# Kernel tuning notes

Measured on AMD Instinct MI355X. Metric: run time of the kernel, lower is better.

## Reference

```python
import jax, jax.numpy as jnp
import numpy as np

B, S, E, H = 4, 8192, 1024, 16
D = E // H  # head_dim = 64


def setup_inputs() -> dict:
    key = jax.random.key(0)
    ks = jax.random.split(key, 9)
    s = 0.02
    return {
        "x": jax.random.normal(ks[0], (B, S, E), dtype=jnp.float32),
        "Wq": jax.random.normal(ks[1], (D, E), dtype=jnp.float32) * s,
        "bq": jax.random.normal(ks[2], (D,), dtype=jnp.float32) * s,
        "Wk": jax.random.normal(ks[3], (D, E), dtype=jnp.float32) * s,
        "bk": jax.random.normal(ks[4], (D,), dtype=jnp.float32) * s,
        "Wv": jax.random.normal(ks[5], (D, E), dtype=jnp.float32) * s,
        "bv": jax.random.normal(ks[6], (D,), dtype=jnp.float32) * s,
        "Wo": jax.random.normal(ks[7], (E, E), dtype=jnp.float32) * s,
        "bo": jax.random.normal(ks[8], (E,), dtype=jnp.float32) * s,
    }


def reference(x, Wq, bq, Wk, bk, Wv, bv, Wo, bo):
    b, s, e = x.shape
    d = Wq.shape[0]          # head_dim (projections map embed_dim -> head_dim)
    h = e // d               # num_heads
    # torch Linear: y = x @ W.T + b ; projected shape [B, S, d]
    # view(B, -1, h, d) on [B, S, d] => effective seq S' = S // h (faithful to source)
    def split_heads(t):
        return t.reshape(b, -1, h, d).transpose(0, 2, 1, 3)  # [B, H, S', D]
    q = split_heads(x @ Wq.T + bq)
    k = split_heads(x @ Wk.T + bk)
    v = split_heads(x @ Wv.T + bv)
    scores = jnp.einsum('bhqd,bhkd->bhqk', q, k) / np.sqrt(d).astype(jnp.float32)
    attn = jax.nn.softmax(scores, axis=-1)  # dropout=0.0 => identity
    ctx = jnp.einsum('bhqk,bhkd->bhqd', attn, v)
    ctx = ctx.transpose(0, 2, 1, 3).reshape(b, -1, e)  # [B, S', E]
    return ctx @ Wo.T + bo
```

## Files before the change

kernel.cpp:

```cpp
#include <hip/hip_runtime.h>
#include <hip/hip_bf16.h>


typedef unsigned short u16;
typedef __attribute__((ext_vector_type(8))) short short8;
typedef __attribute__((ext_vector_type(4))) float f32x4;

#define VMWAIT(N) asm volatile("s_waitcnt vmcnt(" #N ")" ::: "memory")
#define MEMFENCE() asm volatile("" ::: "memory")
#define BAR() __builtin_amdgcn_s_barrier()

__device__ inline u16 f2bf(float f) {
    union { float f; unsigned u; } v; v.f = f;
    unsigned u = v.u;
    return (u16)((u + 0x7fffu + ((u >> 16) & 1u)) >> 16);
}
__device__ inline unsigned pack_bf2(float a, float b) {
    union { __hip_bfloat162 h; unsigned u; } v;
    v.h = __float22bfloat162_rn(float2{a, b});
    return v.u;
}
__device__ __forceinline__ void gld16(void* lds, const void* gptr) {
    __builtin_amdgcn_global_load_lds(
        (const __attribute__((address_space(1))) unsigned int*)gptr,
        (__attribute__((address_space(3))) unsigned int*)lds,
        16, 0, 0);
}

__global__ __launch_bounds__(256) void convw(
    const float* __restrict__ Wq, const float* __restrict__ bq,
    const float* __restrict__ Wk, const float* __restrict__ bk,
    const float* __restrict__ Wv, const float* __restrict__ bv,
    const float* __restrict__ Wo,
    u16* __restrict__ Wqkv, float* __restrict__ qkvb, u16* __restrict__ Wob)
{
    const int idx = blockIdx.x * 256 + threadIdx.x;
    Wob[idx] = f2bf(Wo[idx]);
    if (idx < 196608) {
        const int row = idx >> 10, k = idx & 1023;
        float v = (row < 64)  ? Wq[row * 1024 + k] * 0.125f
                : (row < 128) ? Wk[(row - 64) * 1024 + k]
                              : Wv[(row - 128) * 1024 + k];
        Wqkv[idx] = f2bf(v);
    }
    if (idx < 192) {
        qkvb[idx] = (idx < 64) ? bq[idx] * 0.125f
                  : (idx < 128) ? bk[idx - 64] : bv[idx - 128];
    }
}

__global__ __launch_bounds__(256) void qkv_gemm(
    const float* __restrict__ X, const u16* __restrict__ W,
    const float* __restrict__ bias, u16* __restrict__ Out)
{
    __shared__ short8 Bs[2][1536];

    const int tid = threadIdx.x;
    const int lane = tid & 63, wid = tid >> 6;
    const int q = lane >> 4, r = lane & 15;
    const long m0 = (long)blockIdx.x * 64;

    const u16* wp[6];
    #pragma unroll
    for (int i = 0; i < 6; ++i) {
        const int p = wid * 6 + i, kk2 = p / 12, nt = p % 12;
        wp[i] = W + (long)(nt * 16 + r) * 1024 + kk2 * 32 + q * 8;
    }

    const float* px = X + (m0 + wid * 16 + r) * 1024 + q * 8;

    f32x4 acc[12] = {};

    #pragma unroll
    for (int i = 0; i < 6; ++i)
        gld16(&Bs[0][(wid * 6 + i) * 64], wp[i]);
    float4 a[4];
    a[0] = *(const float4*)(px);
    a[1] = *(const float4*)(px + 4);
    a[2] = *(const float4*)(px + 32);
    a[3] = *(const float4*)(px + 36);

    for (int k0 = 0; k0 < 1024; k0 += 64) {
        const int buf = (k0 >> 6) & 1;
        float4 an[4] = {};
        if (k0 + 64 < 1024) {
            #pragma unroll
            for (int i = 0; i < 6; ++i)
                gld16(&Bs[buf ^ 1][(wid * 6 + i) * 64], wp[i] + k0 + 64);
            an[0] = *(const float4*)(px + k0 + 64);
            an[1] = *(const float4*)(px + k0 + 68);
            an[2] = *(const float4*)(px + k0 + 96);
            an[3] = *(const float4*)(px + k0 + 100);
            VMWAIT(10);
        } else {
            VMWAIT(0);
        }
        BAR();
        MEMFENCE();
        #pragma unroll
        for (int kk2 = 0; kk2 < 2; ++kk2) {
            union { short8 s; unsigned u[4]; } af;
            af.u[0] = pack_bf2(a[kk2 * 2].x, a[kk2 * 2].y);
            af.u[1] = pack_bf2(a[kk2 * 2].z, a[kk2 * 2].w);
            af.u[2] = pack_bf2(a[kk2 * 2 + 1].x, a[kk2 * 2 + 1].y);
            af.u[3] = pack_bf2(a[kk2 * 2 + 1].z, a[kk2 * 2 + 1].w);
            #pragma unroll
            for (int nt = 0; nt < 12; ++nt)
                acc[nt] = __builtin_amdgcn_mfma_f32_16x16x32_bf16(
                    af.s, Bs[buf][(kk2 * 12 + nt) * 64 + lane], acc[nt], 0, 0, 0);
        }
        MEMFENCE();
        BAR();
        #pragma unroll
        for (int i = 0; i < 4; ++i) a[i] = an[i];
    }

    u16* reg = (u16*)(&Bs[0][0]) + wid * 3072;
    #pragma unroll
    for (int nt = 0; nt < 12; ++nt) {
        const float badd = bias[nt * 16 + r];
        #pragma unroll
        for (int e = 0; e < 4; ++e)
            reg[(q * 4 + e) * 192 + nt * 16 + r] = f2bf(acc[nt][e] + badd);
    }
    asm volatile("s_waitcnt lgkmcnt(0)" ::: "memory");
    u16* ob = Out + (m0 + wid * 16) * 192;
    #pragma unroll
    for (int t = 0; t < 6; ++t) {
        short8 v = *(const short8*)(reg + t * 512 + lane * 8);
        *(short8*)(ob + t * 512 + lane * 8) = v;
    }
}

__global__ __launch_bounds__(256) void vtrans(
    const u16* __restrict__ qkv, u16* __restrict__ Vt)
{
    __shared__ u16 T[64][68];
    const int bh = blockIdx.x, b = bh >> 4, h = bh & 15;
    const int i0 = blockIdx.y * 64;
    const int tid = threadIdx.x;

    #pragma unroll
    for (int it = 0; it < 2; ++it) {
        const int c = tid + 256 * it;
        const int il = c >> 3, d8 = (c & 7) * 8;
        short8 v = *(const short8*)(qkv +
            ((long)b * 8192 + (long)(i0 + il) * 16 + h) * 192 + 128 + d8);
        #pragma unroll
        for (int j = 0; j < 8; ++j) T[d8 + j][il] = (u16)v[j];
    }
    __syncthreads();
    #pragma unroll
    for (int it = 0; it < 2; ++it) {
        const int c = tid + 256 * it;
        const int dl = c >> 3, i8 = (c & 7) * 8;
        short8 o;
        #pragma unroll
        for (int j = 0; j < 8; ++j) o[j] = (short)T[dl][i8 + j];
        *(short8*)(Vt + ((long)bh * 64 + dl) * 512 + i0 + i8) = o;
    }
}

__global__ __launch_bounds__(256) void attn_flash(
    const u16* __restrict__ qkv, const u16* __restrict__ Vt,
    u16* __restrict__ ctx)
{
    __shared__ short8 Ks[2][512];
    __shared__ short8 Vs[2][512];
    __shared__ u16 Plds[4][16 * 72];

    const int tid = threadIdx.x, lane = tid & 63, wid = tid >> 6;
    const int q = lane >> 4, r = lane & 15;
    const int qt = blockIdx.x;
    const int bh = blockIdx.y;
    const int b = bh >> 4, h = bh & 15;
    const long qrowbase = (long)b * 8192 + h;

    short8 Qf0, Qf1;
    {
        const int i = qt * 64 + wid * 16 + r;
        const u16* p = qkv + (qrowbase + (long)i * 16) * 192 + q * 8;
        Qf0 = *(const short8*)(p);
        Qf1 = *(const short8*)(p + 32);
    }

    const u16* kbase = qkv + (qrowbase + (long)(wid * 16 + r) * 16) * 192
                           + 64 + q * 8;
    const u16* vbase = Vt + ((long)bh * 64 + wid * 16 + r) * 512 + q * 8;

    gld16(&Ks[0][wid * 64],       kbase);
    gld16(&Ks[0][256 + wid * 64], kbase + 32);
    gld16(&Vs[0][wid * 64],       vbase);
    gld16(&Vs[0][256 + wid * 64], vbase + 32);

    f32x4 O[4] = {};
    float mrun = -1e30f, lrun = 0.f;
    u16* Pw = &Plds[wid][0];

    for (int c = 0; c < 8; ++c) {
        const int j0 = c * 64, buf = c & 1;
        if (c < 7) {
            const u16* kp = kbase + (long)(j0 + 64) * 3072;
            const u16* vp = vbase + j0 + 64;
            gld16(&Ks[buf ^ 1][wid * 64],       kp);
            gld16(&Ks[buf ^ 1][256 + wid * 64], kp + 32);
            gld16(&Vs[buf ^ 1][wid * 64],       vp);
            gld16(&Vs[buf ^ 1][256 + wid * 64], vp + 32);
            VMWAIT(4);
        } else {
            VMWAIT(0);
        }
        BAR();
        MEMFENCE();
        f32x4 S[4];
        #pragma unroll
        for (int ct = 0; ct < 4; ++ct) {
            f32x4 s = {};
            s = __builtin_amdgcn_mfma_f32_16x16x32_bf16(
                Ks[buf][ct * 64 + lane], Qf0, s, 0, 0, 0);
            s = __builtin_amdgcn_mfma_f32_16x16x32_bf16(
                Ks[buf][256 + ct * 64 + lane], Qf1, s, 0, 0, 0);
            S[ct] = s;
        }
        float mc = -1e30f;
        #pragma unroll
        for (int ct = 0; ct < 4; ++ct)
            mc = fmaxf(mc, fmaxf(fmaxf(S[ct][0], S[ct][1]),
                                 fmaxf(S[ct][2], S[ct][3])));
        mc = fmaxf(mc, __shfl_xor(mc, 16, 64));
        mc = fmaxf(mc, __shfl_xor(mc, 32, 64));
        const float mnew = fmaxf(mrun, mc);
        const float alpha = __expf(mrun - mnew);
        mrun = mnew;
        float se = 0.f;
        #pragma unroll
        for (int ct = 0; ct < 4; ++ct)
            #pragma unroll
            for (int e = 0; e < 4; ++e) {
                const float pv = __expf(S[ct][e] - mnew);
                S[ct][e] = pv; se += pv;
            }
        se += __shfl_xor(se, 16, 64);
        se += __shfl_xor(se, 32, 64);
        lrun = lrun * alpha + se;
        #pragma unroll
        for (int nt = 0; nt < 4; ++nt)
            #pragma unroll
            for (int e = 0; e < 4; ++e) O[nt][e] *= alpha;
        #pragma unroll
        for (int ct = 0; ct < 4; ++ct) {
            uint2 d;
            d.x = pack_bf2(S[ct][0], S[ct][1]);
            d.y = pack_bf2(S[ct][2], S[ct][3]);
            *(uint2*)(Pw + r * 72 + ct * 16 + q * 4) = d;
        }
        short8 Pf0 = *(const short8*)(Pw + r * 72 + q * 8);
        short8 Pf1 = *(const short8*)(Pw + r * 72 + 32 + q * 8);
        #pragma unroll
        for (int nt = 0; nt < 4; ++nt) {
            O[nt] = __builtin_amdgcn_mfma_f32_16x16x32_bf16(
                Vs[buf][nt * 64 + lane], Pf0, O[nt], 0, 0, 0);
            O[nt] = __builtin_amdgcn_mfma_f32_16x16x32_bf16(
                Vs[buf][256 + nt * 64 + lane], Pf1, O[nt], 0, 0, 0);
        }
        MEMFENCE();
        BAR();
    }

    const float inv = 1.0f / lrun;
    const long i = qt * 64 + wid * 16 + r;
    u16* po = ctx + ((long)b * 512 + i) * 1024 + h * 64;
    #pragma unroll
    for (int nt = 0; nt < 4; ++nt) {
        uint2 d;
        d.x = pack_bf2(O[nt][0] * inv, O[nt][1] * inv);
        d.y = pack_bf2(O[nt][2] * inv, O[nt][3] * inv);
        *(uint2*)(po + nt * 16 + q * 4) = d;
    }
}

__global__ __launch_bounds__(256) void gemm_o(
    const u16* __restrict__ A, const u16* __restrict__ B,
    const float* __restrict__ bias, float* __restrict__ C)
{
    __shared__ short8 As[2][512];
    __shared__ short8 Bs[2][512];

    const int tid = threadIdx.x;
    const int lane = tid & 63, wid = tid >> 6;
    const int q = lane >> 4, r = lane & 15;
    const long m0 = (long)blockIdx.x * 64, n0 = (long)blockIdx.y * 64;
    const int wm = wid >> 1, wn = wid & 1;

    const u16* ap[2];
    const u16* bp[2];
    #pragma unroll
    for (int i = 0; i < 2; ++i) {
        const int t = wid * 2 + i, f = t >> 2, mt = t & 3;
        ap[i] = A + (m0 + mt * 16 + r) * 1024 + f * 32 + q * 8;
        bp[i] = B + (n0 + mt * 16 + r) * 1024 + f * 32 + q * 8;
    }

    #pragma unroll
    for (int i = 0; i < 2; ++i) {
        gld16(&As[0][(wid * 2 + i) * 64], ap[i]);
        gld16(&Bs[0][(wid * 2 + i) * 64], bp[i]);
    }

    f32x4 acc[2][2] = {};

    for (int k0 = 0; k0 < 1024; k0 += 64) {
        const int buf = (k0 >> 6) & 1;
        if (k0 + 64 < 1024) {
            #pragma unroll
            for (int i = 0; i < 2; ++i) {
                gld16(&As[buf ^ 1][(wid * 2 + i) * 64], ap[i] + k0 + 64);
                gld16(&Bs[buf ^ 1][(wid * 2 + i) * 64], bp[i] + k0 + 64);
            }
            VMWAIT(4);
        } else {
            VMWAIT(0);
        }
        BAR();
        MEMFENCE();
        #pragma unroll
        for (int f = 0; f < 2; ++f) {
            short8 af0 = As[buf][f * 256 + (wm * 2 + 0) * 64 + lane];
            short8 af1 = As[buf][f * 256 + (wm * 2 + 1) * 64 + lane];
            short8 bf0 = Bs[buf][f * 256 + (wn * 2 + 0) * 64 + lane];
            short8 bf1 = Bs[buf][f * 256 + (wn * 2 + 1) * 64 + lane];
            acc[0][0] = __builtin_amdgcn_mfma_f32_16x16x32_bf16(af0, bf0, acc[0][0], 0, 0, 0);
            acc[0][1] = __builtin_amdgcn_mfma_f32_16x16x32_bf16(af0, bf1, acc[0][1], 0, 0, 0);
            acc[1][0] = __builtin_amdgcn_mfma_f32_16x16x32_bf16(af1, bf0, acc[1][0], 0, 0, 0);
            acc[1][1] = __builtin_amdgcn_mfma_f32_16x16x32_bf16(af1, bf1, acc[1][1], 0, 0, 0);
        }
        MEMFENCE();
        BAR();
    }

    #pragma unroll
    for (int i = 0; i < 2; ++i)
        #pragma unroll
        for (int j = 0; j < 2; ++j) {
            const long col = n0 + (wn * 2 + j) * 16 + r;
            const float badd = bias[col];
            #pragma unroll
            for (int e = 0; e < 4; ++e) {
                const long row = m0 + (wm * 2 + i) * 16 + q * 4 + e;
                C[row * 1024 + col] = acc[i][j][e] + badd;
            }
        }
}

extern "C" void kernel_launch(void* const* d_in, const int* in_sizes, int n_in,
                              void* d_out, int out_size, void* d_ws, size_t ws_size,
                              hipStream_t stream)
{
    const float* x  = (const float*)d_in[0];
    const float* Wq = (const float*)d_in[1];
    const float* bq = (const float*)d_in[2];
    const float* Wk = (const float*)d_in[3];
    const float* bk = (const float*)d_in[4];
    const float* Wv = (const float*)d_in[5];
    const float* bv = (const float*)d_in[6];
    const float* Wo = (const float*)d_in[7];
    const float* bo = (const float*)d_in[8];
    float* out = (float*)d_out;
    char* ws = (char*)d_ws;

    u16*   qkv  = (u16*)(ws);
    u16*   Vt   = (u16*)(ws + 12582912);
    u16*   Wqkv = (u16*)(ws + 16777216);
    u16*   Wob  = (u16*)(ws + 17170432);
    float* qkvb = (float*)(ws + 19267584);
    u16*   ctx  = (u16*)(ws + 19268352);

    convw<<<4096, 256, 0, stream>>>(Wq, bq, Wk, bk, Wv, bv, Wo, Wqkv, qkvb, Wob);
    qkv_gemm<<<512, 256, 0, stream>>>(x, Wqkv, qkvb, qkv);
    vtrans<<<dim3(64, 8), 256, 0, stream>>>(qkv, Vt);
    attn_flash<<<dim3(8, 64), 256, 0, stream>>>(qkv, Vt, ctx);
    gemm_o<<<dim3(32, 16), 256, 0, stream>>>(ctx, Wob, bo, out);
}
```

Measured before the change: 261.2 us.

## Retile QKV GEMM waves into 2x2 grid to halve LDS B-fragment reads

Each wave now computes a 32-row by 96-column tile instead of 16 rows by 192 columns. Every B fragment read from LDS now feeds two MFMAs, which halves LDS read traffic per MFMA. In exchange each wave loads twice as many X rows, so the vmcnt wait count grows and the per-wave X global load volume doubles. The epilogue now writes the whole block tile to shared memory and stores it after a barrier.

Result: no change. 265.9 us (+1.8%).

```diff
diff --git a/kernel.cpp b/kernel.cpp
--- a/kernel.cpp
+++ b/kernel.cpp
@@ -58,6 +58,7 @@
     const int tid = threadIdx.x;
     const int lane = tid & 63, wid = tid >> 6;
     const int q = lane >> 4, r = lane & 15;
+    const int wm = wid >> 1, wn = wid & 1;
     const long m0 = (long)blockIdx.x * 64;
 
     const u16* wp[6];
@@ -67,31 +68,42 @@
         wp[i] = W + (long)(nt * 16 + r) * 1024 + kk2 * 32 + q * 8;
     }
 
-    const float* px = X + (m0 + wid * 16 + r) * 1024 + q * 8;
-
-    f32x4 acc[12] = {};
-
+    const float* px0 = X + (m0 + wm * 32 + r) * 1024 + q * 8;
+    const float* px1 = px0 + 16 * 1024;
+
+    f32x4 acc[2][6] = {};
+
+    float4 a[2][4];
+    a[0][0] = *(const float4*)(px0);
+    a[0][1] = *(const float4*)(px0 + 4);
+    a[0][2] = *(const float4*)(px0 + 32);
+    a[0][3] = *(const float4*)(px0 + 36);
+    a[1][0] = *(const float4*)(px1);
+    a[1][1] = *(const float4*)(px1 + 4);
+    a[1][2] = *(const float4*)(px1 + 32);
+    a[1][3] = *(const float4*)(px1 + 36);
+    MEMFENCE();
     #pragma unroll
     for (int i = 0; i < 6; ++i)
         gld16(&Bs[0][(wid * 6 + i) * 64], wp[i]);
-    float4 a[4];
-    a[0] = *(const float4*)(px);
-    a[1] = *(const float4*)(px + 4);
-    a[2] = *(const float4*)(px + 32);
-    a[3] = *(const float4*)(px + 36);
 
     for (int k0 = 0; k0 < 1024; k0 += 64) {
         const int buf = (k0 >> 6) & 1;
-        float4 an[4] = {};
+        float4 an[2][4];
         if (k0 + 64 < 1024) {
+            an[0][0] = *(const float4*)(px0 + k0 + 64);
+            an[0][1] = *(const float4*)(px0 + k0 + 68);
+            an[0][2] = *(const float4*)(px0 + k0 + 96);
+            an[0][3] = *(const float4*)(px0 + k0 + 100);
+            an[1][0] = *(const float4*)(px1 + k0 + 64);
+            an[1][1] = *(const float4*)(px1 + k0 + 68);
+            an[1][2] = *(const float4*)(px1 + k0 + 96);
+            an[1][3] = *(const float4*)(px1 + k0 + 100);
+            MEMFENCE();
             #pragma unroll
             for (int i = 0; i < 6; ++i)
                 gld16(&Bs[buf ^ 1][(wid * 6 + i) * 64], wp[i] + k0 + 64);
-            an[0] = *(const float4*)(px + k0 + 64);
-            an[1] = *(const float4*)(px + k0 + 68);
-            an[2] = *(const float4*)(px + k0 + 96);
-            an[3] = *(const float4*)(px + k0 + 100);
-            VMWAIT(10);
+            VMWAIT(14);
         } else {
             VMWAIT(0);
         }
@@ -99,36 +111,54 @@
         MEMFENCE();
         #pragma unroll
         for (int kk2 = 0; kk2 < 2; ++kk2) {
-            union { short8 s; unsigned u[4]; } af;
-            af.u[0] = pack_bf2(a[kk2 * 2].x, a[kk2 * 2].y);
-            af.u[1] = pack_bf2(a[kk2 * 2].z, a[kk2 * 2].w);
-            af.u[2] = pack_bf2(a[kk2 * 2 + 1].x, a[kk2 * 2 + 1].y);
-            af.u[3] = pack_bf2(a[kk2 * 2 + 1].z, a[kk2 * 2 + 1].w);
-            #pragma unroll
-            for (int nt = 0; nt < 12; ++nt)
-                acc[nt] = __builtin_amdgcn_mfma_f32_16x16x32_bf16(
-                    af.s, Bs[buf][(kk2 * 12 + nt) * 64 + lane], acc[nt], 0, 0, 0);
-        }
-        MEMFENCE();
-        BAR();
-        #pragma unroll
-        for (int i = 0; i < 4; ++i) a[i] = an[i];
-    }
-
-    u16* reg = (u16*)(&Bs[0][0]) + wid * 3072;
-    #pragma unroll
-    for (int nt = 0; nt < 12; ++nt) {
-        const float badd = bias[nt * 16 + r];
-        #pragma unroll
-        for (int e = 0; e < 4; ++e)
-            reg[(q * 4 + e) * 192 + nt * 16 + r] = f2bf(acc[nt][e] + badd);
+            union { short8 s; unsigned u[4]; } af0, af1;
+            af0.u[0] = pack_bf2(a[0][kk2 * 2].x, a[0][kk2 * 2].y);
+            af0.u[1] = pack_bf2(a[0][kk2 * 2].z, a[0][kk2 * 2].w);
+            af0.u[2] = pack_bf2(a[0][kk2 * 2 + 1].x, a[0][kk2 * 2 + 1].y);
+            af0.u[3] = pack_bf2(a[0][kk2 * 2 + 1].z, a[0][kk2 * 2 + 1].w);
+            af1.u[0] = pack_bf2(a[1][kk2 * 2].x, a[1][kk2 * 2].y);
+            af1.u[1] = pack_bf2(a[1][kk2 * 2].z, a[1][kk2 * 2].w);
+            af1.u[2] = pack_bf2(a[1][kk2 * 2 + 1].x, a[1][kk2 * 2 + 1].y);
+            af1.u[3] = pack_bf2(a[1][kk2 * 2 + 1].z, a[1][kk2 * 2 + 1].w);
+            #pragma unroll
+            for (int j = 0; j < 6; ++j) {
+                const short8 bf = Bs[buf][(kk2 * 12 + wn * 6 + j) * 64 + lane];
+                acc[0][j] = __builtin_amdgcn_mfma_f32_16x16x32_bf16(
+                    af0.s, bf, acc[0][j], 0, 0, 0);
+                acc[1][j] = __builtin_amdgcn_mfma_f32_16x16x32_bf16(
+                    af1.s, bf, acc[1][j], 0, 0, 0);
+            }
+        }
+        MEMFENCE();
+        BAR();
+        if (k0 + 64 < 1024) {
+            #pragma unroll
+            for (int mf = 0; mf < 2; ++mf)
+                #pragma unroll
+                for (int i = 0; i < 4; ++i) a[mf][i] = an[mf][i];
+        }
+    }
+
+    u16* lds0 = (u16*)&Bs[0][0];
+    #pragma unroll
+    for (int j = 0; j < 6; ++j) {
+        const int col = wn * 96 + j * 16 + r;
+        const float badd = bias[col];
+        #pragma unroll
+        for (int mf = 0; mf < 2; ++mf)
+            #pragma unroll
+            for (int e = 0; e < 4; ++e)
+                lds0[(wm * 32 + mf * 16 + q * 4 + e) * 192 + col] =
+                    f2bf(acc[mf][j][e] + badd);
     }
     asm volatile("s_waitcnt lgkmcnt(0)" ::: "memory");
-    u16* ob = Out + (m0 + wid * 16) * 192;
-    #pragma unroll
-    for (int t = 0; t < 6; ++t) {
-        short8 v = *(const short8*)(reg + t * 512 + lane * 8);
-        *(short8*)(ob + t * 512 + lane * 8) = v;
+    BAR();
+    const short8* l8 = (const short8*)lds0;
+    u16* ob = Out + m0 * 192;
+    #pragma unroll
+    for (int s = 0; s < 6; ++s) {
+        short8 v = l8[tid + s * 256];
+        *(short8*)(ob + (long)(tid + s * 256) * 8) = v;
     }
 }
 
```
